# Performance work log

Hardware: AMD Instinct MI355X
Metric: run time of the kernel (lower is better)

Reference implementation:

```python
import jax, jax.numpy as jnp
import numpy as np

N_NODES = 10000
N_EDGES = 160000
N_FEATS = 9       # OGB atom features
VOCAB = 128       # >= max atom feature cardinality (119)
D = 128           # d_input == d_atom_emb
H = 4             # n_heads
C = 128           # out_channels per head (== d_input)
L = 3             # n_layers
N_CLASSES = 10
NEG_SLOPE = 0.2   # PyG GATConv default


def setup_inputs() -> dict:
    key = jax.random.key(0)
    ks = jax.random.split(key, 10)
    nodes_features = jax.random.randint(ks[0], (N_NODES, N_FEATS), 0, 119, dtype=jnp.int64)
    edges_connectivity = jax.random.randint(ks[1], (2, N_EDGES), 0, N_NODES, dtype=jnp.int64)
    s = 1.0 / np.sqrt(D)
    emb_tables = jax.random.normal(ks[2], (N_FEATS, VOCAB, D), dtype=jnp.float32) * s
    W = jax.random.normal(ks[3], (L, D, H * C), dtype=jnp.float32) * s
    att_src = jax.random.normal(ks[4], (L, H, C), dtype=jnp.float32) * s
    att_dst = jax.random.normal(ks[5], (L, H, C), dtype=jnp.float32) * s
    bias = jnp.zeros((L, C), dtype=jnp.float32)
    Wc = jax.random.normal(ks[6], (D, N_CLASSES), dtype=jnp.float32) * s
    bc = jnp.zeros((N_CLASSES,), dtype=jnp.float32)
    return {"nodes_features": nodes_features, "edges_connectivity": edges_connectivity,
            "emb_tables": emb_tables, "W": W, "att_src": att_src, "att_dst": att_dst,
            "bias": bias, "Wc": Wc, "bc": bc}


def _gat_layer(x, src, dst, W_l, a_s, a_d, b_l):
    # x: [N, D] -> h: [N, H, C]
    h = (x @ W_l).reshape(-1, H, C)
    alpha_src = jnp.einsum('nhc,hc->nh', h, a_s)  # [N, H]
    alpha_dst = jnp.einsum('nhc,hc->nh', h, a_d)  # [N, H]
    e = alpha_src[src] + alpha_dst[dst]           # [E, H]
    e = jnp.where(e >= 0, e, NEG_SLOPE * e)       # LeakyReLU(0.2)
    # segment softmax over edges grouped by destination node
    m = jax.ops.segment_max(e, dst, num_segments=N_NODES)  # [N, H]
    ex = jnp.exp(e - m[dst])
    s = jax.ops.segment_sum(ex, dst, num_segments=N_NODES)  # [N, H]
    alpha = ex / (s[dst] + 1e-16)                 # [E, H]
    msg = h[src] * alpha[..., None]               # [E, H, C]
    out = jax.ops.segment_sum(msg, dst, num_segments=N_NODES)  # [N, H, C]
    return out.mean(axis=1) + b_l                 # concat=False: mean over heads


def reference(nodes_features, edges_connectivity, emb_tables, W, att_src, att_dst, bias, Wc, bc):
    # AtomEncoder: sum per-feature embeddings -> [N, D]
    x = emb_tables[jnp.arange(N_FEATS), nodes_features].sum(axis=1)
    src, dst = edges_connectivity[0], edges_connectivity[1]
    for i in range(L):
        # dropout treated as identity (eval-mode reference)
        x = _gat_layer(x, src, dst, W[i], att_src[i], att_dst[i], bias[i])
        if i < L - 1:
            x = jax.nn.gelu(x)
    pooled = x.mean(axis=0)                       # graph mean-pool over nodes -> [D]
    return pooled @ Wc + bc                       # [n_classes]
```

## Files before the change

kernel.cpp:

```cpp
#include <hip/hip_runtime.h>
#include <hip/hip_bf16.h>
#include <math.h>

#define NN 10000
#define NE 160000
#define NF 9
#define VOCAB 128
#define D 128
#define NH 4
#define C 128
#define HC 512
#define NCLS 10
#define NL 3

typedef __attribute__((ext_vector_type(8))) short bf16x8;
typedef __attribute__((ext_vector_type(4))) float f32x4;

__device__ __forceinline__ unsigned short f2bf(float f) {
    unsigned u = __float_as_uint(f);
    unsigned r = ((u >> 16) & 1u) + 0x7FFFu;
    return (unsigned short)((u + r) >> 16);
}
__device__ __forceinline__ float bf2f(unsigned short h) {
    return __uint_as_float(((unsigned)h) << 16);
}
__device__ __forceinline__ void fsplit(float v, unsigned short* hi, unsigned short* lo) {
    unsigned short h = f2bf(v);
    *hi = h;
    *lo = f2bf(v - bf2f(h));
}

__global__ __launch_bounds__(128)
void atom_encoder(const int* __restrict__ feats, const float* __restrict__ emb,
                  float* __restrict__ x) {
    int n = blockIdx.x;
    int d = threadIdx.x;
    __shared__ int f[NF];
    if (threadIdx.x < NF) f[threadIdx.x] = feats[n * NF + threadIdx.x];
    __syncthreads();
    float acc = 0.f;
#pragma unroll
    for (int i = 0; i < NF; ++i)
        acc += emb[(i * VOCAB + f[i]) * D + d];
    x[n * D + d] = acc;
}

__global__ __launch_bounds__(256)
void hist(const int* __restrict__ dst, int* __restrict__ deg) {
    int e = blockIdx.x * 256 + threadIdx.x;
    if (e < NE) atomicAdd(&deg[dst[e]], 1);
}

#define SCAN_T 1024
#define SCAN_PER ((NN + SCAN_T - 1) / SCAN_T)
__global__ __launch_bounds__(SCAN_T)
void scan_deg(const int* __restrict__ deg, int* __restrict__ rowstart,
              int* __restrict__ cursor) {
    __shared__ int part[SCAN_T];
    int t = threadIdx.x;
    int base = t * SCAN_PER;
    int vals[SCAN_PER];
    int loc = 0;
#pragma unroll
    for (int i = 0; i < SCAN_PER; ++i) {
        int idx = base + i;
        int v = (idx < NN) ? deg[idx] : 0;
        vals[i] = v;
        loc += v;
    }
    part[t] = loc;
    __syncthreads();
    for (int off = 1; off < SCAN_T; off <<= 1) {
        int y = (t >= off) ? part[t - off] : 0;
        __syncthreads();
        part[t] += y;
        __syncthreads();
    }
    int run = part[t] - loc;
#pragma unroll
    for (int i = 0; i < SCAN_PER; ++i) {
        int idx = base + i;
        if (idx < NN) { rowstart[idx] = run; cursor[idx] = run; }
        run += vals[i];
    }
}

__global__ __launch_bounds__(256)
void scatter(const int* __restrict__ src, const int* __restrict__ dst,
             int* __restrict__ cursor, int* __restrict__ csr_src) {
    int e = blockIdx.x * 256 + threadIdx.x;
    if (e < NE) {
        int p = atomicAdd(&cursor[dst[e]], 1);
        csr_src[p] = src[e];
    }
}

__global__ __launch_bounds__(128)
void prep_att(const float* __restrict__ W, const float* __restrict__ as_,
              const float* __restrict__ ad_, float* __restrict__ wsrc,
              float* __restrict__ wdst) {
    int l = blockIdx.x >> 3;
    int r = blockIdx.x & 7;
    int h = r >> 1;
    int side = r & 1;
    int k = threadIdx.x;
    const float* av = (side ? ad_ : as_) + (size_t)(l * NH + h) * C;
    const float* wrow = W + (size_t)l * D * HC + (size_t)k * HC + h * C;
    float acc = 0.f;
#pragma unroll 4
    for (int c = 0; c < C; ++c) acc += wrow[c] * av[c];
    float* o = (side ? wdst : wsrc) + (size_t)(l * NH + h) * D + k;
    *o = acc;
}

__global__ __launch_bounds__(512)
void prep_w(const float* __restrict__ W, unsigned short* __restrict__ Bth,
            unsigned short* __restrict__ Btl) {
    int l = blockIdx.x >> 7;
    int c = blockIdx.x & 127;
    int j = threadIdx.x;
    float v = W[(size_t)l * D * HC + (size_t)(j & 127) * HC + (j >> 7) * C + c];
    unsigned short h, lo;
    fsplit(v, &h, &lo);
    size_t o = (size_t)(l * 128 + c) * HC + j;
    Bth[o] = h;
    Btl[o] = lo;
}

__global__ __launch_bounds__(256)
void alphas2(const float* __restrict__ X, const float* __restrict__ wsrc,
             const float* __restrict__ wdst, float* __restrict__ asrc,
             float* __restrict__ adst) {
    int n = blockIdx.x * 4 + (threadIdx.x >> 6);
    int lane = threadIdx.x & 63;
    float x0 = X[n * D + lane], x1 = X[n * D + lane + 64];
#pragma unroll
    for (int h = 0; h < NH; ++h) {
        float s = x0 * wsrc[h * D + lane] + x1 * wsrc[h * D + lane + 64];
        float d = x0 * wdst[h * D + lane] + x1 * wdst[h * D + lane + 64];
#pragma unroll
        for (int off = 32; off; off >>= 1) {
            s += __shfl_down(s, off);
            d += __shfl_down(d, off);
        }
        if (lane == 0) { asrc[n * NH + h] = s; adst[n * NH + h] = d; }
    }
}

__global__ __launch_bounds__(128)
void gat_agg(const int* __restrict__ csr_src, const int* __restrict__ rowstart,
             const int* __restrict__ degA, const float* __restrict__ asr,
             const float* __restrict__ adr, const float* __restrict__ X,
             unsigned short* __restrict__ aggh, unsigned short* __restrict__ aggl) {
    int n = blockIdx.x;
    int t = threadIdx.x;
    int deg = degA[n];
    int start = rowstart[n];

    __shared__ float smax[NH];
    __shared__ float sinv[NH];
    __shared__ float lal[128][NH];
    __shared__ int lsrc[128];

    int h = t >> 5, i = t & 31;
    float ad_h = adr[n * NH + h];
    float mx = -INFINITY;
    for (int j = i; j < deg; j += 32) {
        int s = csr_src[start + j];
        float v = asr[s * NH + h] + ad_h;
        v = v >= 0.f ? v : 0.2f * v;
        mx = fmaxf(mx, v);
    }
#pragma unroll
    for (int off = 16; off; off >>= 1) mx = fmaxf(mx, __shfl_xor(mx, off));
    if (i == 0) smax[h] = mx;
    __syncthreads();
    float m = smax[h];
    float ss = 0.f;
    for (int j = i; j < deg; j += 32) {
        int s = csr_src[start + j];
        float v = asr[s * NH + h] + ad_h;
        v = v >= 0.f ? v : 0.2f * v;
        ss += __expf(v - m);
    }
#pragma unroll
    for (int off = 16; off; off >>= 1) ss += __shfl_xor(ss, off);
    if (i == 0) sinv[h] = 0.25f / (ss + 1e-16f);
    __syncthreads();

    float m0 = smax[0], m1 = smax[1], m2 = smax[2], m3 = smax[3];
    float i0 = sinv[0], i1 = sinv[1], i2 = sinv[2], i3 = sinv[3];
    float a0 = adr[n * NH + 0], a1 = adr[n * NH + 1];
    float a2 = adr[n * NH + 2], a3 = adr[n * NH + 3];
    float acc0 = 0.f, acc1 = 0.f, acc2 = 0.f, acc3 = 0.f;

    for (int cb = 0; cb < deg; cb += 128) {
        int cl = deg - cb; if (cl > 128) cl = 128;
        if (t < cl) {
            int s = csr_src[start + cb + t];
            float4 av = *(const float4*)(asr + s * NH);
            float v0 = av.x + a0; v0 = v0 >= 0.f ? v0 : 0.2f * v0;
            float v1 = av.y + a1; v1 = v1 >= 0.f ? v1 : 0.2f * v1;
            float v2 = av.z + a2; v2 = v2 >= 0.f ? v2 : 0.2f * v2;
            float v3 = av.w + a3; v3 = v3 >= 0.f ? v3 : 0.2f * v3;
            lal[t][0] = __expf(v0 - m0) * i0;
            lal[t][1] = __expf(v1 - m1) * i1;
            lal[t][2] = __expf(v2 - m2) * i2;
            lal[t][3] = __expf(v3 - m3) * i3;
            lsrc[t] = s;
        }
        __syncthreads();
#pragma unroll 4
        for (int j = 0; j < cl; ++j) {
            float xv = X[(size_t)lsrc[j] * D + t];
            float4 w = *(const float4*)lal[j];
            acc0 += w.x * xv;
            acc1 += w.y * xv;
            acc2 += w.z * xv;
            acc3 += w.w * xv;
        }
        __syncthreads();
    }

    size_t base = (size_t)n * HC + t;
    unsigned short hh, ll;
    fsplit(acc0, &hh, &ll); aggh[base + 0 * D] = hh; aggl[base + 0 * D] = ll;
    fsplit(acc1, &hh, &ll); aggh[base + 1 * D] = hh; aggl[base + 1 * D] = ll;
    fsplit(acc2, &hh, &ll); aggh[base + 2 * D] = hh; aggl[base + 2 * D] = ll;
    fsplit(acc3, &hh, &ll); aggh[base + 3 * D] = hh; aggl[base + 3 * D] = ll;
}

__global__ __launch_bounds__(64)
void gemm_mfma(const unsigned short* __restrict__ Ah, const unsigned short* __restrict__ Al,
               const unsigned short* __restrict__ Bth, const unsigned short* __restrict__ Btl,
               const float* __restrict__ bias, float* __restrict__ Out, int do_gelu) {
    int lane = threadIdx.x;
    int m0 = blockIdx.x * 16;
    int n0 = blockIdx.y * 64;
    int r = lane & 15;
    int g = lane >> 4;

    const bf16x8* ah = (const bf16x8*)(Ah + (size_t)(m0 + r) * HC + g * 8);
    const bf16x8* al = (const bf16x8*)(Al + (size_t)(m0 + r) * HC + g * 8);
    const bf16x8* bh0 = (const bf16x8*)(Bth + (size_t)(n0 + 0 * 16 + r) * HC + g * 8);
    const bf16x8* bh1 = (const bf16x8*)(Bth + (size_t)(n0 + 1 * 16 + r) * HC + g * 8);
    const bf16x8* bh2 = (const bf16x8*)(Bth + (size_t)(n0 + 2 * 16 + r) * HC + g * 8);
    const bf16x8* bh3 = (const bf16x8*)(Bth + (size_t)(n0 + 3 * 16 + r) * HC + g * 8);
    const bf16x8* bl0 = (const bf16x8*)(Btl + (size_t)(n0 + 0 * 16 + r) * HC + g * 8);
    const bf16x8* bl1 = (const bf16x8*)(Btl + (size_t)(n0 + 1 * 16 + r) * HC + g * 8);
    const bf16x8* bl2 = (const bf16x8*)(Btl + (size_t)(n0 + 2 * 16 + r) * HC + g * 8);
    const bf16x8* bl3 = (const bf16x8*)(Btl + (size_t)(n0 + 3 * 16 + r) * HC + g * 8);

    f32x4 acc[4];
#pragma unroll
    for (int q = 0; q < 4; ++q) acc[q] = (f32x4){0.f, 0.f, 0.f, 0.f};

#pragma unroll 2
    for (int ks = 0; ks < HC / 32; ++ks) {
        bf16x8 a_h = ah[ks * 4];
        bf16x8 a_l = al[ks * 4];
        bf16x8 b;
        b = bh0[ks * 4];
        acc[0] = __builtin_amdgcn_mfma_f32_16x16x32_bf16(a_h, b, acc[0], 0, 0, 0);
        acc[0] = __builtin_amdgcn_mfma_f32_16x16x32_bf16(a_l, b, acc[0], 0, 0, 0);
        b = bl0[ks * 4];
        acc[0] = __builtin_amdgcn_mfma_f32_16x16x32_bf16(a_h, b, acc[0], 0, 0, 0);
        b = bh1[ks * 4];
        acc[1] = __builtin_amdgcn_mfma_f32_16x16x32_bf16(a_h, b, acc[1], 0, 0, 0);
        acc[1] = __builtin_amdgcn_mfma_f32_16x16x32_bf16(a_l, b, acc[1], 0, 0, 0);
        b = bl1[ks * 4];
        acc[1] = __builtin_amdgcn_mfma_f32_16x16x32_bf16(a_h, b, acc[1], 0, 0, 0);
        b = bh2[ks * 4];
        acc[2] = __builtin_amdgcn_mfma_f32_16x16x32_bf16(a_h, b, acc[2], 0, 0, 0);
        acc[2] = __builtin_amdgcn_mfma_f32_16x16x32_bf16(a_l, b, acc[2], 0, 0, 0);
        b = bl2[ks * 4];
        acc[2] = __builtin_amdgcn_mfma_f32_16x16x32_bf16(a_h, b, acc[2], 0, 0, 0);
        b = bh3[ks * 4];
        acc[3] = __builtin_amdgcn_mfma_f32_16x16x32_bf16(a_h, b, acc[3], 0, 0, 0);
        acc[3] = __builtin_amdgcn_mfma_f32_16x16x32_bf16(a_l, b, acc[3], 0, 0, 0);
        b = bl3[ks * 4];
        acc[3] = __builtin_amdgcn_mfma_f32_16x16x32_bf16(a_h, b, acc[3], 0, 0, 0);
    }

#pragma unroll
    for (int q = 0; q < 4; ++q) {
#pragma unroll
        for (int i = 0; i < 4; ++i) {
            int row = m0 + g * 4 + i;
            int col = n0 + q * 16 + r;
            float v = acc[q][i] + bias[col];
            if (do_gelu) {
                float u = 0.7978845608028654f * (v + 0.044715f * v * v * v);
                v = 0.5f * v * (1.f + tanhf(u));
            }
            Out[(size_t)row * D + col] = v;
        }
    }
}

__global__ __launch_bounds__(512)
void pool512(const unsigned short* __restrict__ Ah, const unsigned short* __restrict__ Al,
             float* __restrict__ p) {
    int t = threadIdx.x;
    int chunk = (NN + gridDim.x - 1) / gridDim.x;
    int n0 = blockIdx.x * chunk;
    int n1 = n0 + chunk; if (n1 > NN) n1 = NN;
    float acc = 0.f;
    for (int n = n0; n < n1; ++n)
        acc += bf2f(Ah[(size_t)n * HC + t]) + bf2f(Al[(size_t)n * HC + t]);
    atomicAdd(p + t, acc);
}

__global__ __launch_bounds__(128)
void final_head(const float* __restrict__ p512, const float* __restrict__ W3,
                const float* __restrict__ bias3, const float* __restrict__ Wc,
                const float* __restrict__ bc, float* __restrict__ out) {
    __shared__ float t128[128];
    int t = threadIdx.x;
    float acc = bias3[t];
    const float inv = 1.0f / NN;
#pragma unroll 4
    for (int j = 0; j < HC; ++j)
        acc += p512[j] * inv * W3[(size_t)(j & 127) * HC + (j >> 7) * C + t];
    t128[t] = acc;
    __syncthreads();
    if (t < NCLS) {
        float o = bc[t];
#pragma unroll 4
        for (int c = 0; c < 128; ++c) o += t128[c] * Wc[c * NCLS + t];
        out[t] = o;
    }
}

extern "C" void kernel_launch(void* const* d_in, const int* in_sizes, int n_in,
                              void* d_out, int out_size, void* d_ws, size_t ws_size,
                              hipStream_t stream) {
    const int*   feats = (const int*)d_in[0];
    const int*   edges = (const int*)d_in[1];
    const float* emb   = (const float*)d_in[2];
    const float* W     = (const float*)d_in[3];
    const float* asrcW = (const float*)d_in[4];
    const float* adstW = (const float*)d_in[5];
    const float* bias  = (const float*)d_in[6];
    const float* Wc    = (const float*)d_in[7];
    const float* bc    = (const float*)d_in[8];
    float* out = (float*)d_out;

    const int* srcp = edges;
    const int* dstp = edges + NE;

    char* ws = (char*)d_ws;
    size_t off = 0;
    unsigned short* aggh = (unsigned short*)(ws + off); off += (size_t)NN * HC * 2;
    unsigned short* aggl = (unsigned short*)(ws + off); off += (size_t)NN * HC * 2;
    float* xb0    = (float*)(ws + off); off += (size_t)NN * D * 4;
    float* xb1    = (float*)(ws + off); off += (size_t)NN * D * 4;
    float* asrc   = (float*)(ws + off); off += (size_t)NN * NH * 4;
    float* adst   = (float*)(ws + off); off += (size_t)NN * NH * 4;
    int*   deg    = (int*)(ws + off);   off += (size_t)NN * 4;
    int*   rowst  = (int*)(ws + off);   off += (size_t)NN * 4;
    int*   cursor = (int*)(ws + off);   off += (size_t)NN * 4;
    int*   csrsrc = (int*)(ws + off);   off += (size_t)NE * 4;
    float* wsrcb  = (float*)(ws + off); off += (size_t)NL * NH * D * 4;
    float* wdstb  = (float*)(ws + off); off += (size_t)NL * NH * D * 4;
    unsigned short* Bth = (unsigned short*)(ws + off); off += (size_t)2 * 128 * HC * 2;
    unsigned short* Btl = (unsigned short*)(ws + off); off += (size_t)2 * 128 * HC * 2;
    float* p512   = (float*)(ws + off); off += HC * 4;

    hipMemsetAsync(deg, 0, (size_t)NN * 4, stream);
    hist<<<(NE + 255) / 256, 256, 0, stream>>>(dstp, deg);
    scan_deg<<<1, SCAN_T, 0, stream>>>(deg, rowst, cursor);
    scatter<<<(NE + 255) / 256, 256, 0, stream>>>(srcp, dstp, cursor, csrsrc);
    prep_att<<<NL * NH * 2, 128, 0, stream>>>(W, asrcW, adstW, wsrcb, wdstb);
    prep_w<<<2 * 128, 512, 0, stream>>>(W, Bth, Btl);

    atom_encoder<<<NN, 128, 0, stream>>>(feats, emb, xb0);

    float* xin = xb0;
    float* xout = xb1;
    for (int l = 0; l < 2; ++l) {
        alphas2<<<NN / 4, 256, 0, stream>>>(xin, wsrcb + (size_t)l * NH * D,
                                            wdstb + (size_t)l * NH * D, asrc, adst);
        gat_agg<<<NN, 128, 0, stream>>>(csrsrc, rowst, deg, asrc, adst, xin, aggh, aggl);
        gemm_mfma<<<dim3(NN / 16, 2), 64, 0, stream>>>(
            aggh, aggl, Bth + (size_t)l * 128 * HC, Btl + (size_t)l * 128 * HC,
            bias + (size_t)l * D, xout, 1);
        float* tmp = xin; xin = xout; xout = tmp;
    }

    alphas2<<<NN / 4, 256, 0, stream>>>(xin, wsrcb + (size_t)2 * NH * D,
                                        wdstb + (size_t)2 * NH * D, asrc, adst);
    gat_agg<<<NN, 128, 0, stream>>>(csrsrc, rowst, deg, asrc, adst, xin, aggh, aggl);
    hipMemsetAsync(p512, 0, HC * 4, stream);
    pool512<<<100, 512, 0, stream>>>(aggh, aggl, p512);
    final_head<<<1, 128, 0, stream>>>(p512, W + (size_t)2 * D * HC,
                                      bias + (size_t)2 * D, Wc, bc, out);
}
```

Baseline: 336.5 us.

## Use online softmax in GAT aggregation, pack agg stores, fold head weights

gat_agg now computes per-head max and sum in one pass using an online-softmax merge across all 128 threads, instead of two separate 32-lane passes over the edge list. The aggregate layout is changed to node-major interleaved heads (j = k*4+h), so each thread writes packed uint2 stores, and prep_w is remapped to match. The final head W3·Wc and its bias are precomputed into a 10x512 matrix, which replaces final_head with a small reduction and removes a memset. This cuts redundant gather traffic and serial head math, at the cost of extra exp calls in the online merge.

Result: faster. 320.1 us (-4.9%).

```diff
diff --git a/kernel.cpp b/kernel.cpp
--- a/kernel.cpp
+++ b/kernel.cpp
@@ -13,6 +13,8 @@
 #define NCLS 10
 #define NL 3
 
+#define NEG_BIG (-1e30f)
+
 typedef __attribute__((ext_vector_type(8))) short bf16x8;
 typedef __attribute__((ext_vector_type(4))) float f32x4;
 
@@ -23,11 +25,6 @@
 }
 __device__ __forceinline__ float bf2f(unsigned short h) {
     return __uint_as_float(((unsigned)h) << 16);
-}
-__device__ __forceinline__ void fsplit(float v, unsigned short* hi, unsigned short* lo) {
-    unsigned short h = f2bf(v);
-    *hi = h;
-    *lo = f2bf(v - bf2f(h));
 }
 
 __global__ __launch_bounds__(128)
@@ -119,12 +116,32 @@
     int l = blockIdx.x >> 7;
     int c = blockIdx.x & 127;
     int j = threadIdx.x;
-    float v = W[(size_t)l * D * HC + (size_t)(j & 127) * HC + (j >> 7) * C + c];
-    unsigned short h, lo;
-    fsplit(v, &h, &lo);
+    float v = W[(size_t)l * D * HC + (size_t)(j >> 2) * HC + (j & 3) * C + c];
+    unsigned short h = f2bf(v);
+    unsigned short lo = f2bf(v - bf2f(h));
     size_t o = (size_t)(l * 128 + c) * HC + j;
     Bth[o] = h;
     Btl[o] = lo;
+}
+
+__global__ __launch_bounds__(512)
+void prep_head(const float* __restrict__ W3, const float* __restrict__ Wc,
+               const float* __restrict__ bias3, const float* __restrict__ bc,
+               float* __restrict__ M, float* __restrict__ b10,
+               float* __restrict__ p512) {
+    int k = blockIdx.x;
+    int j = threadIdx.x;
+    const float* wrow = W3 + (size_t)(j >> 2) * HC + (j & 3) * C;
+    float acc = 0.f;
+#pragma unroll 4
+    for (int c = 0; c < C; ++c) acc += wrow[c] * Wc[c * NCLS + k];
+    M[(size_t)k * HC + j] = acc;
+    if (k == 0) p512[j] = 0.f;
+    if (j == 0) {
+        float b = bc[k];
+        for (int c = 0; c < C; ++c) b += bias3[c] * Wc[c * NCLS + k];
+        b10[k] = b;
+    }
 }
 
 __global__ __launch_bounds__(256)
@@ -151,63 +168,79 @@
 void gat_agg(const int* __restrict__ csr_src, const int* __restrict__ rowstart,
              const int* __restrict__ degA, const float* __restrict__ asr,
              const float* __restrict__ adr, const float* __restrict__ X,
-             unsigned short* __restrict__ aggh, unsigned short* __restrict__ aggl) {
+             unsigned* __restrict__ aggh, unsigned* __restrict__ aggl) {
     int n = blockIdx.x;
     int t = threadIdx.x;
     int deg = degA[n];
     int start = rowstart[n];
 
-    __shared__ float smax[NH];
-    __shared__ float sinv[NH];
+    __shared__ float redm[2][NH];
+    __shared__ float reds[2][NH];
     __shared__ float lal[128][NH];
     __shared__ int lsrc[128];
 
-    int h = t >> 5, i = t & 31;
-    float ad_h = adr[n * NH + h];
-    float mx = -INFINITY;
-    for (int j = i; j < deg; j += 32) {
-        int s = csr_src[start + j];
-        float v = asr[s * NH + h] + ad_h;
-        v = v >= 0.f ? v : 0.2f * v;
-        mx = fmaxf(mx, v);
-    }
-#pragma unroll
-    for (int off = 16; off; off >>= 1) mx = fmaxf(mx, __shfl_xor(mx, off));
-    if (i == 0) smax[h] = mx;
-    __syncthreads();
-    float m = smax[h];
-    float ss = 0.f;
-    for (int j = i; j < deg; j += 32) {
-        int s = csr_src[start + j];
-        float v = asr[s * NH + h] + ad_h;
-        v = v >= 0.f ? v : 0.2f * v;
-        ss += __expf(v - m);
-    }
-#pragma unroll
-    for (int off = 16; off; off >>= 1) ss += __shfl_xor(ss, off);
-    if (i == 0) sinv[h] = 0.25f / (ss + 1e-16f);
-    __syncthreads();
-
-    float m0 = smax[0], m1 = smax[1], m2 = smax[2], m3 = smax[3];
-    float i0 = sinv[0], i1 = sinv[1], i2 = sinv[2], i3 = sinv[3];
     float a0 = adr[n * NH + 0], a1 = adr[n * NH + 1];
     float a2 = adr[n * NH + 2], a3 = adr[n * NH + 3];
+
+    float m[NH] = {NEG_BIG, NEG_BIG, NEG_BIG, NEG_BIG};
+    float s[NH] = {0.f, 0.f, 0.f, 0.f};
+    for (int j = t; j < deg; j += 128) {
+        int sn = csr_src[start + j];
+        float4 av = *(const float4*)(asr + sn * NH);
+        float v[NH];
+        v[0] = av.x + a0; v[0] = v[0] >= 0.f ? v[0] : 0.2f * v[0];
+        v[1] = av.y + a1; v[1] = v[1] >= 0.f ? v[1] : 0.2f * v[1];
+        v[2] = av.z + a2; v[2] = v[2] >= 0.f ? v[2] : 0.2f * v[2];
+        v[3] = av.w + a3; v[3] = v[3] >= 0.f ? v[3] : 0.2f * v[3];
+#pragma unroll
+        for (int h = 0; h < NH; ++h) {
+            float nm = fmaxf(m[h], v[h]);
+            s[h] = s[h] * __expf(m[h] - nm) + __expf(v[h] - nm);
+            m[h] = nm;
+        }
+    }
+#pragma unroll
+    for (int off = 32; off; off >>= 1) {
+#pragma unroll
+        for (int h = 0; h < NH; ++h) {
+            float om = __shfl_xor(m[h], off);
+            float os = __shfl_xor(s[h], off);
+            float nm = fmaxf(m[h], om);
+            s[h] = s[h] * __expf(m[h] - nm) + os * __expf(om - nm);
+            m[h] = nm;
+        }
+    }
+    if ((t & 63) == 0) {
+        int w = t >> 6;
+#pragma unroll
+        for (int h = 0; h < NH; ++h) { redm[w][h] = m[h]; reds[w][h] = s[h]; }
+    }
+    __syncthreads();
+    float fm[NH], fi[NH];
+#pragma unroll
+    for (int h = 0; h < NH; ++h) {
+        float m0 = redm[0][h], m1 = redm[1][h];
+        float nm = fmaxf(m0, m1);
+        float sv = reds[0][h] * __expf(m0 - nm) + reds[1][h] * __expf(m1 - nm);
+        fm[h] = nm;
+        fi[h] = 0.25f / (sv + 1e-16f);
+    }
+
     float acc0 = 0.f, acc1 = 0.f, acc2 = 0.f, acc3 = 0.f;
-
     for (int cb = 0; cb < deg; cb += 128) {
         int cl = deg - cb; if (cl > 128) cl = 128;
         if (t < cl) {
-            int s = csr_src[start + cb + t];
-            float4 av = *(const float4*)(asr + s * NH);
+            int sn = csr_src[start + cb + t];
+            float4 av = *(const float4*)(asr + sn * NH);
             float v0 = av.x + a0; v0 = v0 >= 0.f ? v0 : 0.2f * v0;
             float v1 = av.y + a1; v1 = v1 >= 0.f ? v1 : 0.2f * v1;
             float v2 = av.z + a2; v2 = v2 >= 0.f ? v2 : 0.2f * v2;
             float v3 = av.w + a3; v3 = v3 >= 0.f ? v3 : 0.2f * v3;
-            lal[t][0] = __expf(v0 - m0) * i0;
-            lal[t][1] = __expf(v1 - m1) * i1;
-            lal[t][2] = __expf(v2 - m2) * i2;
-            lal[t][3] = __expf(v3 - m3) * i3;
-            lsrc[t] = s;
+            lal[t][0] = __expf(v0 - fm[0]) * fi[0];
+            lal[t][1] = __expf(v1 - fm[1]) * fi[1];
+            lal[t][2] = __expf(v2 - fm[2]) * fi[2];
+            lal[t][3] = __expf(v3 - fm[3]) * fi[3];
+            lsrc[t] = sn;
         }
         __syncthreads();
 #pragma unroll 4
@@ -222,12 +255,16 @@
         __syncthreads();
     }
 
-    size_t base = (size_t)n * HC + t;
-    unsigned short hh, ll;
-    fsplit(acc0, &hh, &ll); aggh[base + 0 * D] = hh; aggl[base + 0 * D] = ll;
-    fsplit(acc1, &hh, &ll); aggh[base + 1 * D] = hh; aggl[base + 1 * D] = ll;
-    fsplit(acc2, &hh, &ll); aggh[base + 2 * D] = hh; aggl[base + 2 * D] = ll;
-    fsplit(acc3, &hh, &ll); aggh[base + 3 * D] = hh; aggl[base + 3 * D] = ll;
+    unsigned short h0 = f2bf(acc0), h1 = f2bf(acc1), h2 = f2bf(acc2), h3 = f2bf(acc3);
+    unsigned short l0 = f2bf(acc0 - bf2f(h0)), l1 = f2bf(acc1 - bf2f(h1));
+    unsigned short l2 = f2bf(acc2 - bf2f(h2)), l3 = f2bf(acc3 - bf2f(h3));
+    size_t base = ((size_t)n * HC + t * 4) >> 1;
+    uint2 uh = make_uint2((unsigned)h0 | ((unsigned)h1 << 16),
+                          (unsigned)h2 | ((unsigned)h3 << 16));
+    uint2 ul = make_uint2((unsigned)l0 | ((unsigned)l1 << 16),
+                          (unsigned)l2 | ((unsigned)l3 << 16));
+    *(uint2*)(aggh + base) = uh;
+    *(uint2*)(aggl + base) = ul;
 }
 
 __global__ __launch_bounds__(64)
@@ -311,25 +348,20 @@
     atomicAdd(p + t, acc);
 }
 
-__global__ __launch_bounds__(128)
-void final_head(const float* __restrict__ p512, const float* __restrict__ W3,
-                const float* __restrict__ bias3, const float* __restrict__ Wc,
-                const float* __restrict__ bc, float* __restrict__ out) {
-    __shared__ float t128[128];
-    int t = threadIdx.x;
-    float acc = bias3[t];
-    const float inv = 1.0f / NN;
-#pragma unroll 4
-    for (int j = 0; j < HC; ++j)
-        acc += p512[j] * inv * W3[(size_t)(j & 127) * HC + (j >> 7) * C + t];
-    t128[t] = acc;
-    __syncthreads();
-    if (t < NCLS) {
-        float o = bc[t];
-#pragma unroll 4
-        for (int c = 0; c < 128; ++c) o += t128[c] * Wc[c * NCLS + t];
-        out[t] = o;
-    }
+__global__ __launch_bounds__(640)
+void final10(const float* __restrict__ p512, const float* __restrict__ M,
+             const float* __restrict__ b10, float* __restrict__ out) {
+    int k = threadIdx.x >> 6;
+    int lane = threadIdx.x & 63;
+    float acc = 0.f;
+#pragma unroll
+    for (int i = 0; i < HC / 64; ++i) {
+        int j = lane + i * 64;
+        acc += p512[j] * M[(size_t)k * HC + j];
+    }
+#pragma unroll
+    for (int off = 32; off; off >>= 1) acc += __shfl_down(acc, off);
+    if (lane == 0) out[k] = b10[k] + acc * (1.0f / NN);
 }
 
 extern "C" void kernel_launch(void* const* d_in, const int* in_sizes, int n_in,
@@ -365,6 +397,8 @@
     float* wdstb  = (float*)(ws + off); off += (size_t)NL * NH * D * 4;
     unsigned short* Bth = (unsigned short*)(ws + off); off += (size_t)2 * 128 * HC * 2;
     unsigned short* Btl = (unsigned short*)(ws + off); off += (size_t)2 * 128 * HC * 2;
+    float* Mhead  = (float*)(ws + off); off += (size_t)NCLS * HC * 4;
+    float* b10    = (float*)(ws + off); off += NCLS * 4;
     float* p512   = (float*)(ws + off); off += HC * 4;
 
     hipMemsetAsync(deg, 0, (size_t)NN * 4, stream);
@@ -373,6 +407,8 @@
     scatter<<<(NE + 255) / 256, 256, 0, stream>>>(srcp, dstp, cursor, csrsrc);
     prep_att<<<NL * NH * 2, 128, 0, stream>>>(W, asrcW, adstW, wsrcb, wdstb);
     prep_w<<<2 * 128, 512, 0, stream>>>(W, Bth, Btl);
+    prep_head<<<NCLS, 512, 0, stream>>>(W + (size_t)2 * D * HC, Wc,
+                                        bias + (size_t)2 * D, bc, Mhead, b10, p512);
 
     atom_encoder<<<NN, 128, 0, stream>>>(feats, emb, xb0);
 
@@ -381,7 +417,8 @@
     for (int l = 0; l < 2; ++l) {
         alphas2<<<NN / 4, 256, 0, stream>>>(xin, wsrcb + (size_t)l * NH * D,
                                             wdstb + (size_t)l * NH * D, asrc, adst);
-        gat_agg<<<NN, 128, 0, stream>>>(csrsrc, rowst, deg, asrc, adst, xin, aggh, aggl);
+        gat_agg<<<NN, 128, 0, stream>>>(csrsrc, rowst, deg, asrc, adst, xin,
+                                        (unsigned*)aggh, (unsigned*)aggl);
         gemm_mfma<<<dim3(NN / 16, 2), 64, 0, stream>>>(
             aggh, aggl, Bth + (size_t)l * 128 * HC, Btl + (size_t)l * 128 * HC,
             bias + (size_t)l * D, xout, 1);
@@ -390,9 +427,8 @@
 
     alphas2<<<NN / 4, 256, 0, stream>>>(xin, wsrcb + (size_t)2 * NH * D,
                                         wdstb + (size_t)2 * NH * D, asrc, adst);
-    gat_agg<<<NN, 128, 0, stream>>>(csrsrc, rowst, deg, asrc, adst, xin, aggh, aggl);
-    hipMemsetAsync(p512, 0, HC * 4, stream);
+    gat_agg<<<NN, 128, 0, stream>>>(csrsrc, rowst, deg, asrc, adst, xin,
+                                    (unsigned*)aggh, (unsigned*)aggl);
     pool512<<<100, 512, 0, stream>>>(aggh, aggl, p512);
-    final_head<<<1, 128, 0, stream>>>(p512, W + (size_t)2 * D * HC,
-                                      bias + (size_t)2 * D, Wc, bc, out);
-}
+    final10<<<1, 640, 0, stream>>>(p512, Mhead, b10, out);
+}
```
